# Performance work log

Measured on AMD Instinct MI355X. Metric: run time of the kernel, lower is better.

The kernel has to match this reference:

```python
import jax, jax.numpy as jnp
import numpy as np

V, E, H, L, S, B = 32000, 512, 1024, 2, 512, 32


def setup_inputs() -> dict:
    key = jax.random.key(0)
    ks = jax.random.split(key, 12)
    s = 0.05  # keep activations in a sane range
    return {
        "x": jax.random.randint(ks[0], (S, B), 0, V),
        "embed": jax.random.normal(ks[1], (V, E), dtype=jnp.float32) * s,
        "W_ih0": jax.random.normal(ks[2], (4 * H, E), dtype=jnp.float32) * s,
        "W_hh0": jax.random.normal(ks[3], (4 * H, H), dtype=jnp.float32) * s,
        "b_ih0": jax.random.normal(ks[4], (4 * H,), dtype=jnp.float32) * s,
        "b_hh0": jax.random.normal(ks[5], (4 * H,), dtype=jnp.float32) * s,
        "W_ih1": jax.random.normal(ks[6], (4 * H, H), dtype=jnp.float32) * s,
        "W_hh1": jax.random.normal(ks[7], (4 * H, H), dtype=jnp.float32) * s,
        "b_ih1": jax.random.normal(ks[8], (4 * H,), dtype=jnp.float32) * s,
        "b_hh1": jax.random.normal(ks[9], (4 * H,), dtype=jnp.float32) * s,
        "h0": jax.random.normal(ks[10], (L, B, H), dtype=jnp.float32) * s,
        "c0": jax.random.normal(ks[11], (L, B, H), dtype=jnp.float32) * s,
    }


def _lstm_cell(x_t, h_prev, c_prev, Wi, Wh, bi, bh):
    # PyTorch gate order: input, forget, cell(g), output
    gates = x_t @ Wi.T + h_prev @ Wh.T + bi + bh  # [B, 4H]
    i, f, g, o = jnp.split(gates, 4, axis=-1)
    i = jax.nn.sigmoid(i)
    f = jax.nn.sigmoid(f)
    g = jnp.tanh(g)
    o = jax.nn.sigmoid(o)
    c_new = f * c_prev + i * g
    h_new = o * jnp.tanh(c_new)
    return h_new, c_new


def reference(x, embed, W_ih0, W_hh0, b_ih0, b_hh0,
              W_ih1, W_hh1, b_ih1, b_hh1, h0, c0):
    emb = embed[x]  # [S, B, E]; dropout p=0.0 -> identity
    layers = ((W_ih0, W_hh0, b_ih0, b_hh0), (W_ih1, W_hh1, b_ih1, b_hh1))

    def step(carry, e_t):
        h, c = carry  # each [L, B, H]
        inp = e_t
        new_h, new_c = [], []
        for l, (Wi, Wh, bi, bh) in enumerate(layers):
            h_l, c_l = _lstm_cell(inp, h[l], c[l], Wi, Wh, bi, bh)
            new_h.append(h_l)
            new_c.append(c_l)
            inp = h_l  # inter-layer dropout p=0.0 -> identity
        h = jnp.stack(new_h)
        c = jnp.stack(new_c)
        return (h, c), (inp, h, c)

    (_, _), (outs, hiddens, cells) = jax.lax.scan(step, (h0, c0), emb)
    outputs = outs[:, None, :, :]  # match torch shape [S, 1, B, H]
    return outputs, hiddens, cells
```

## Files before the change

kernel.cpp:

```cpp
#include <hip/hip_runtime.h>
#include <hip/hip_cooperative_groups.h>

namespace cg = cooperative_groups;


#define S_LEN 512
#define BATCH 32
#define HID   1024
#define EMB   512
#define NBLK  128
#define NTHR  512

typedef short  bf16x8 __attribute__((ext_vector_type(8)));
typedef float  f32x4  __attribute__((ext_vector_type(4)));

union U8 { bf16x8 v; unsigned short us[8]; uint4 u4; unsigned long long ull[2]; };

__device__ __forceinline__ unsigned short f2bf(float f) {
    unsigned u = __float_as_uint(f);
    u += 0x7fffu + ((u >> 16) & 1u);
    return (unsigned short)(u >> 16);
}

__device__ __forceinline__ uint4 pack8(float4 lo, float4 hi) {
    U8 r;
    r.us[0] = f2bf(lo.x); r.us[1] = f2bf(lo.y); r.us[2] = f2bf(lo.z); r.us[3] = f2bf(lo.w);
    r.us[4] = f2bf(hi.x); r.us[5] = f2bf(hi.y); r.us[6] = f2bf(hi.z); r.us[7] = f2bf(hi.w);
    return r.u4;
}

__device__ __forceinline__ f32x4 mfma16(bf16x8 a, bf16x8 b, f32x4 c) {
    return __builtin_amdgcn_mfma_f32_16x16x32_bf16(a, b, c, 0, 0, 0);
}

__device__ __forceinline__ U8 ld_ws16(const uint4* p) {
    const unsigned long long* q = (const unsigned long long*)p;
    U8 r;
    r.ull[0] = __hip_atomic_load(q,     __ATOMIC_RELAXED, __HIP_MEMORY_SCOPE_AGENT);
    r.ull[1] = __hip_atomic_load(q + 1, __ATOMIC_RELAXED, __HIP_MEMORY_SCOPE_AGENT);
    return r;
}
__device__ __forceinline__ void st_ws16(uint4* p, U8 v) {
    unsigned long long* q = (unsigned long long*)p;
    __hip_atomic_store(q,     v.ull[0], __ATOMIC_RELAXED, __HIP_MEMORY_SCOPE_AGENT);
    __hip_atomic_store(q + 1, v.ull[1], __ATOMIC_RELAXED, __HIP_MEMORY_SCOPE_AGENT);
}

__device__ __forceinline__ float sigm(float x) {
    return __builtin_amdgcn_rcpf(1.0f + __expf(-x));
}
__device__ __forceinline__ float tanh_fast(float x) {
    const float xc = fminf(fmaxf(x, -15.f), 15.f);
    const float t  = __expf(2.f * xc);
    return (t - 1.f) * __builtin_amdgcn_rcpf(t + 1.f);
}

__device__ __forceinline__ void poll64(const int* flags, int target) {
    const int* p = flags + ((threadIdx.x & 63) << 4);
    for (;;) {
        const int v = __hip_atomic_load(p, __ATOMIC_RELAXED, __HIP_MEMORY_SCOPE_AGENT);
        if (__all(v >= target)) break;
        __builtin_amdgcn_s_sleep(1);
    }
}
__device__ __forceinline__ void pollsub(const int* flags, int base, int cnt, int target) {
    const int l   = threadIdx.x & 63;
    const int idx = (l < cnt) ? l : 0;
    const int* p  = flags + ((base + idx) << 4);
    for (;;) {
        const int v = __hip_atomic_load(p, __ATOMIC_RELAXED, __HIP_MEMORY_SCOPE_AGENT);
        if (__all(v >= target)) break;
        __builtin_amdgcn_s_sleep(1);
    }
}

__global__ __launch_bounds__(NTHR, 1)
void lstm_pipe(const int* __restrict__ x, const float* __restrict__ embed,
               const float* __restrict__ Wi0, const float* __restrict__ Wh0,
               const float* __restrict__ bi0, const float* __restrict__ bh0,
               const float* __restrict__ Wi1, const float* __restrict__ Wh1,
               const float* __restrict__ bi1, const float* __restrict__ bh1,
               const float* __restrict__ h0in, const float* __restrict__ c0in,
               float* __restrict__ outputs, float* __restrict__ hiddens,
               float* __restrict__ cells, uint4* __restrict__ ws)
{
    __shared__ f32x4 sRed[8][8][64];
    __shared__ uint4 sEmb[64 * 33];
    __shared__ float sGates[32][68];
    __shared__ unsigned short sHex[32][16];
    __shared__ float sBias[16][4];

    const int tid  = threadIdx.x;
    const int lane = tid & 63;
    const int wv   = tid >> 6;
    const int bx   = blockIdx.x;
    const bool isL0 = (bx < 64);
    const int g    = isL0 ? bx : bx - 64;

    uint4* h0base = ws;
    uint4* h1base = ws + 16384;
    int*   fbase  = (int*)(ws + 24576);
    int*   flag0  = fbase;
    int*   flag1  = fbase + 1024;

    {
        const int gt = bx * NTHR + tid;
        if (gt < 2048) fbase[gt] = 0;
        if (gt < 8192) {
            const int layer = gt >> 12, kg = (gt >> 5) & 127, b = gt & 31;
            const float* src = h0in + (((size_t)layer << 5) + b) * HID + (kg << 3);
            uint4* dst = layer ? (h1base + 4096) : (h0base + 3 * 4096);
            dst[(kg << 5) + b] = pack8(*(const float4*)src, *(const float4*)(src + 4));
        }
    }
    if (tid < 16) {
        #pragma unroll
        for (int gate = 0; gate < 4; ++gate) {
            const int r = (gate << 10) + (g << 4) + tid;
            sBias[tid][gate] = isL0 ? (bi0[r] + bh0[r]) : (bi1[r] + bh1[r]);
        }
    }
    const int pjj = tid & 15;
    const int pb  = tid >> 4;
    const int jg  = (g << 4) + pjj;
    float creg = isL0 ? c0in[(size_t)pb * HID + jg]
                      : c0in[(size_t)(BATCH + pb) * HID + jg];

    const int n_  = lane & 15;
    const int ko_ = (lane >> 4) << 3;
    const int rb_ = ((n_ >> 2) << 10) + (g << 4) + (n_ & 3);
    bf16x8 w0[4][6];
    bf16x8 w1[4][8];
    if (isL0) {
        #pragma unroll
        for (int nt = 0; nt < 4; ++nt) {
            const int r = rb_ + (nt << 2);
            #pragma unroll
            for (int kf = 0; kf < 6; ++kf) {
                const int k = wv * 192 + kf * 32 + ko_;
                const float* src = (k < EMB) ? Wi0 + (size_t)r * EMB + k
                                             : Wh0 + (size_t)r * HID + (k - EMB);
                U8 t; t.u4 = pack8(*(const float4*)src, *(const float4*)(src + 4));
                w0[nt][kf] = t.v;
            }
        }
    } else {
        #pragma unroll
        for (int nt = 0; nt < 4; ++nt) {
            const int r = rb_ + (nt << 2);
            #pragma unroll
            for (int kf = 0; kf < 8; ++kf) {
                const int k = (wv << 8) + kf * 32 + ko_;
                const float* src = (k < HID) ? Wi1 + (size_t)r * HID + k
                                             : Wh1 + (size_t)r * HID + (k - HID);
                U8 t; t.u4 = pack8(*(const float4*)src, *(const float4*)(src + 4));
                w1[nt][kf] = t.v;
            }
        }
    }

    float4 pe[4][2];
    if (isL0) {
        #pragma unroll
        for (int it = 0; it < 4; ++it) {
            const int b = wv + (it << 3);
            const float* src = embed + (size_t)x[b] * EMB + (lane << 3);
            sEmb[lane * 33 + b] = pack8(*(const float4*)src, *(const float4*)(src + 4));
        }
        #pragma unroll
        for (int it = 0; it < 4; ++it) {
            const int b = wv + (it << 3);
            const float* src = embed + (size_t)x[32 + b] * EMB + (lane << 3);
            pe[it][0] = *(const float4*)src;
            pe[it][1] = *(const float4*)(src + 4);
        }
    }

    cg::grid_group grid = cg::this_grid();
    grid.sync();

    const size_t BH = (size_t)BATCH * HID;

    if (isL0) {
        for (int s = 0; s < S_LEN; ++s) {
            U8 r0[6], r1[6];
            if (wv >= 2) {
                const int fst = (wv * 6 < 16) ? 16 : wv * 6;
                const int pb0 = (fst - 16) << 1;
                const int pct = ((wv * 6 + 6 - 16) << 1) - pb0;
                pollsub(flag0, pb0, pct, s);
                const uint4* h0p = h0base + (((s + 3) & 3) << 12);
                #pragma unroll
                for (int kf = 0; kf < 6; ++kf) {
                    const int kfg = wv * 6 + kf;
                    if (kfg >= 16) {
                        const int u = (((kfg - 16) << 2) + (lane >> 4)) * 32 + (lane & 15);
                        r0[kf] = ld_ws16(&h0p[u]);
                        r1[kf] = ld_ws16(&h0p[u + 16]);
                    }
                }
            }
            f32x4 acc[2][4] = {{{0,0,0,0},{0,0,0,0},{0,0,0,0},{0,0,0,0}},
                               {{0,0,0,0},{0,0,0,0},{0,0,0,0},{0,0,0,0}}};
            #pragma unroll
            for (int kf = 0; kf < 6; ++kf) {
                const int kfg = wv * 6 + kf;
                bf16x8 a0, a1;
                if (kfg < 16) {
                    const int u = ((kfg << 2) + (lane >> 4)) * 33 + (lane & 15);
                    U8 t0; t0.u4 = sEmb[u];      a0 = t0.v;
                    U8 t1; t1.u4 = sEmb[u + 16]; a1 = t1.v;
                } else {
                    a0 = r0[kf].v;
                    a1 = r1[kf].v;
                }
                #pragma unroll
                for (int nt = 0; nt < 4; ++nt) {
                    acc[0][nt] = mfma16(a0, w0[nt][kf], acc[0][nt]);
                    acc[1][nt] = mfma16(a1, w0[nt][kf], acc[1][nt]);
                }
            }
            #pragma unroll
            for (int mt = 0; mt < 2; ++mt)
                #pragma unroll
                for (int nt = 0; nt < 4; ++nt)
                    sRed[wv][(mt << 2) + nt][lane] = acc[mt][nt];
            __syncthreads();

            if (s + 1 < S_LEN) {
                #pragma unroll
                for (int it = 0; it < 4; ++it)
                    sEmb[lane * 33 + wv + (it << 3)] = pack8(pe[it][0], pe[it][1]);
            }
            if (s + 2 < S_LEN) {
                #pragma unroll
                for (int it = 0; it < 4; ++it) {
                    const int b = wv + (it << 3);
                    const float* src = embed + (size_t)x[((s + 2) << 5) + b] * EMB + (lane << 3);
                    pe[it][0] = *(const float4*)src;
                    pe[it][1] = *(const float4*)(src + 4);
                }
            }
            {
                const int tile = tid >> 6, l = tid & 63;
                f32x4 sum = sRed[0][tile][l];
                #pragma unroll
                for (int w = 1; w < 8; ++w) sum += sRed[w][tile][l];
                const int mt = tile >> 2, nt = tile & 3;
                const int b0 = (mt << 4) + ((l >> 4) << 2);
                const int col = (nt << 4) + (l & 15);
                sGates[b0 + 0][col] = sum[0];
                sGates[b0 + 1][col] = sum[1];
                sGates[b0 + 2][col] = sum[2];
                sGates[b0 + 3][col] = sum[3];
            }
            __syncthreads();

            float cn_out, hn_out;
            {
                const int cb = ((pjj >> 2) << 4) + (pjj & 3);
                const float ii = sigm     (sGates[pb][cb]      + sBias[pjj][0]);
                const float ff = sigm     (sGates[pb][cb + 4]  + sBias[pjj][1]);
                const float gg = tanh_fast(sGates[pb][cb + 8]  + sBias[pjj][2]);
                const float oo = sigm     (sGates[pb][cb + 12] + sBias[pjj][3]);
                cn_out = ff * creg + ii * gg;
                creg = cn_out;
                hn_out = oo * tanh_fast(cn_out);
                sHex[pb][pjj] = f2bf(hn_out);
            }
            __syncthreads();

            if (wv == 0) {
                if (s >= 4) poll64(flag1, s - 3);
                const int b = lane & 31, kgl = lane >> 5;
                U8 hb;
                #pragma unroll
                for (int jj = 0; jj < 8; ++jj) hb.us[jj] = sHex[b][(kgl << 3) + jj];
                st_ws16(h0base + ((s & 3) << 12) + (((g << 1) + kgl) << 5) + b, hb);
                asm volatile("s_waitcnt vmcnt(0)" ::: "memory");
                if (lane == 0)
                    __hip_atomic_store(flag0 + (g << 4), s + 1,
                                       __ATOMIC_RELAXED, __HIP_MEMORY_SCOPE_AGENT);
            }
            cells  [(size_t)(s << 1) * BH + (size_t)pb * HID + jg] = cn_out;
            hiddens[(size_t)(s << 1) * BH + (size_t)pb * HID + jg] = hn_out;
        }
    } else {
        for (int s = 0; s < S_LEN; ++s) {
            if (wv < 4) pollsub(flag0, wv << 4, 16, s + 1);
            else        poll64(flag1, s);

            const uint4* h0c = h0base + ((s & 3) << 12);
            const uint4* h1p = h1base + (((s + 1) & 1) << 12);
            U8 r0[8], r1[8];
            #pragma unroll
            for (int kf = 0; kf < 8; ++kf) {
                const int kfg = (wv << 3) + kf;
                const uint4* src = (kfg < 32) ? h0c : h1p;
                const int u = (((kfg & 31) << 2) + (lane >> 4)) * 32 + (lane & 15);
                r0[kf] = ld_ws16(&src[u]);
                r1[kf] = ld_ws16(&src[u + 16]);
            }
            f32x4 acc[2][4] = {{{0,0,0,0},{0,0,0,0},{0,0,0,0},{0,0,0,0}},
                               {{0,0,0,0},{0,0,0,0},{0,0,0,0},{0,0,0,0}}};
            #pragma unroll
            for (int kf = 0; kf < 8; ++kf) {
                #pragma unroll
                for (int nt = 0; nt < 4; ++nt) {
                    acc[0][nt] = mfma16(r0[kf].v, w1[nt][kf], acc[0][nt]);
                    acc[1][nt] = mfma16(r1[kf].v, w1[nt][kf], acc[1][nt]);
                }
            }
            #pragma unroll
            for (int mt = 0; mt < 2; ++mt)
                #pragma unroll
                for (int nt = 0; nt < 4; ++nt)
                    sRed[wv][(mt << 2) + nt][lane] = acc[mt][nt];
            __syncthreads();
            {
                const int tile = tid >> 6, l = tid & 63;
                f32x4 sum = sRed[0][tile][l];
                #pragma unroll
                for (int w = 1; w < 8; ++w) sum += sRed[w][tile][l];
                const int mt = tile >> 2, nt = tile & 3;
                const int b0 = (mt << 4) + ((l >> 4) << 2);
                const int col = (nt << 4) + (l & 15);
                sGates[b0 + 0][col] = sum[0];
                sGates[b0 + 1][col] = sum[1];
                sGates[b0 + 2][col] = sum[2];
                sGates[b0 + 3][col] = sum[3];
            }
            __syncthreads();
            float cn_out, hn_out;
            {
                const int cb = ((pjj >> 2) << 4) + (pjj & 3);
                const float ii = sigm     (sGates[pb][cb]      + sBias[pjj][0]);
                const float ff = sigm     (sGates[pb][cb + 4]  + sBias[pjj][1]);
                const float gg = tanh_fast(sGates[pb][cb + 8]  + sBias[pjj][2]);
                const float oo = sigm     (sGates[pb][cb + 12] + sBias[pjj][3]);
                cn_out = ff * creg + ii * gg;
                creg = cn_out;
                hn_out = oo * tanh_fast(cn_out);
                sHex[pb][pjj] = f2bf(hn_out);
            }
            __syncthreads();
            if (wv == 0) {
                const int b = lane & 31, kgl = lane >> 5;
                U8 hb;
                #pragma unroll
                for (int jj = 0; jj < 8; ++jj) hb.us[jj] = sHex[b][(kgl << 3) + jj];
                st_ws16(h1base + ((s & 1) << 12) + (((g << 1) + kgl) << 5) + b, hb);
                asm volatile("s_waitcnt vmcnt(0)" ::: "memory");
                if (lane == 0)
                    __hip_atomic_store(flag1 + (g << 4), s + 1,
                                       __ATOMIC_RELAXED, __HIP_MEMORY_SCOPE_AGENT);
            }
            {
                const size_t o = (size_t)pb * HID + jg;
                cells  [(size_t)((s << 1) + 1) * BH + o] = cn_out;
                hiddens[(size_t)((s << 1) + 1) * BH + o] = hn_out;
                outputs[(size_t)s * BH + o]              = hn_out;
            }
        }
    }
}

#define KC 256
__global__ __launch_bounds__(256)
void lstm_step(const float* __restrict__ Wi, const float* __restrict__ Wh,
               const float* __restrict__ bi, const float* __restrict__ bh,
               const float* __restrict__ xsrc, const int* __restrict__ xidx, int K1,
               const float* __restrict__ Hprev, const float* __restrict__ Cprev,
               float* __restrict__ Hout, float* __restrict__ Cout,
               float* __restrict__ Hout2)
{
    __shared__ float As[32][KC + 4];
    __shared__ float red[256][5];

    const int t  = threadIdx.x;
    const int b  = t & 31;
    const int jl = (t >> 5) & 1;
    const int ks = t >> 6;
    const int j  = (blockIdx.x << 1) + jl;

    const int Ktot = K1 + HID;
    const int NC   = Ktot / KC;

    float acc0 = 0.f, acc1 = 0.f, acc2 = 0.f, acc3 = 0.f;

    for (int c = 0; c < NC; ++c) {
        const int  k0  = c * KC;
        const bool isX = (k0 < K1);

        #pragma unroll
        for (int i = 0; i < 8; ++i) {
            const int idx4 = t + (i << 8);
            const int row  = idx4 >> 6;
            const int c4   = idx4 & 63;
            const float* src;
            if (isX) {
                const size_t r0 = xidx ? (size_t)xidx[row] : (size_t)row;
                src = xsrc + r0 * (size_t)K1 + k0;
            } else {
                src = Hprev + (size_t)row * HID + (k0 - K1);
            }
            *(float4*)&As[row][c4 << 2] = *(const float4*)(src + (c4 << 2));
        }
        __syncthreads();

        const float* W      = isX ? Wi : Wh;
        const int    stride = isX ? K1 : HID;
        const int    kw     = k0 + (ks << 6) - (isX ? 0 : K1);
        const float* w0 = W + (size_t)(j       ) * stride + kw;
        const float* w1 = W + (size_t)(j + 1024) * stride + kw;
        const float* w2 = W + (size_t)(j + 2048) * stride + kw;
        const float* w3 = W + (size_t)(j + 3072) * stride + kw;
        const float* a  = &As[b][ks << 6];

        #pragma unroll 4
        for (int kk = 0; kk < 64; kk += 4) {
            const float4 av = *(const float4*)(a + kk);
            float4 w;
            w = *(const float4*)(w0 + kk);
            acc0 = fmaf(av.x, w.x, acc0); acc0 = fmaf(av.y, w.y, acc0);
            acc0 = fmaf(av.z, w.z, acc0); acc0 = fmaf(av.w, w.w, acc0);
            w = *(const float4*)(w1 + kk);
            acc1 = fmaf(av.x, w.x, acc1); acc1 = fmaf(av.y, w.y, acc1);
            acc1 = fmaf(av.z, w.z, acc1); acc1 = fmaf(av.w, w.w, acc1);
            w = *(const float4*)(w2 + kk);
            acc2 = fmaf(av.x, w.x, acc2); acc2 = fmaf(av.y, w.y, acc2);
            acc2 = fmaf(av.z, w.z, acc2); acc2 = fmaf(av.w, w.w, acc2);
            w = *(const float4*)(w3 + kk);
            acc3 = fmaf(av.x, w.x, acc3); acc3 = fmaf(av.y, w.y, acc3);
            acc3 = fmaf(av.z, w.z, acc3); acc3 = fmaf(av.w, w.w, acc3);
        }
        __syncthreads();
    }

    red[t][0] = acc0; red[t][1] = acc1; red[t][2] = acc2; red[t][3] = acc3;
    __syncthreads();

    if (t < 64) {
        float tot[4];
        #pragma unroll
        for (int gg = 0; gg < 4; ++gg) {
            const int r = j + (gg << 10);
            tot[gg] = red[t][gg] + red[t + 64][gg] + red[t + 128][gg] + red[t + 192][gg]
                   + bi[r] + bh[r];
        }
        const float ig = 1.f / (1.f + expf(-tot[0]));
        const float fg = 1.f / (1.f + expf(-tot[1]));
        const float gv = tanhf(tot[2]);
        const float og = 1.f / (1.f + expf(-tot[3]));
        const size_t o  = (size_t)b * HID + j;
        const float  cp = Cprev[o];
        const float  cn = fg * cp + ig * gv;
        const float  hn = og * tanhf(cn);
        Cout[o] = cn;
        Hout[o] = hn;
        if (Hout2) Hout2[o] = hn;
    }
}

extern "C" void kernel_launch(void* const* d_in, const int* in_sizes, int n_in,
                              void* d_out, int out_size, void* d_ws, size_t ws_size,
                              hipStream_t stream)
{
    (void)in_sizes; (void)n_in; (void)out_size;

    const int*   x     = (const int*)  d_in[0];
    const float* embed = (const float*)d_in[1];
    const float* Wi0   = (const float*)d_in[2];
    const float* Wh0   = (const float*)d_in[3];
    const float* bi0   = (const float*)d_in[4];
    const float* bh0   = (const float*)d_in[5];
    const float* Wi1   = (const float*)d_in[6];
    const float* Wh1   = (const float*)d_in[7];
    const float* bi1   = (const float*)d_in[8];
    const float* bh1   = (const float*)d_in[9];
    const float* h0in  = (const float*)d_in[10];
    const float* c0in  = (const float*)d_in[11];

    float* out     = (float*)d_out;
    const size_t BH = (size_t)BATCH * HID;
    float* outputs = out;
    float* hiddens = out + (size_t)S_LEN * BH;
    float* cells   = out + 3 * (size_t)S_LEN * BH;
    uint4* ws      = (uint4*)d_ws;

    bool coop_ok = (ws_size >= 401408);
    if (coop_ok) {
        void* args[] = {
            (void*)&x, (void*)&embed,
            (void*)&Wi0, (void*)&Wh0, (void*)&bi0, (void*)&bh0,
            (void*)&Wi1, (void*)&Wh1, (void*)&bi1, (void*)&bh1,
            (void*)&h0in, (void*)&c0in,
            (void*)&outputs, (void*)&hiddens, (void*)&cells, (void*)&ws
        };
        hipError_t e = hipLaunchCooperativeKernel((void*)lstm_pipe,
                                                  dim3(NBLK), dim3(NTHR), args, 0, stream);
        if (e != hipSuccess) { (void)hipGetLastError(); coop_ok = false; }
    }
    if (!coop_ok) {
        for (int s = 0; s < S_LEN; ++s) {
            const float* Hp0 = s ? hiddens + ((size_t)(s - 1) * 2 + 0) * BH : h0in;
            const float* Cp0 = s ? cells   + ((size_t)(s - 1) * 2 + 0) * BH : c0in;
            float* H0o = hiddens + ((size_t)s * 2 + 0) * BH;
            float* C0o = cells   + ((size_t)s * 2 + 0) * BH;
            lstm_step<<<512, 256, 0, stream>>>(Wi0, Wh0, bi0, bh0,
                                               embed, x + (size_t)s * BATCH, EMB,
                                               Hp0, Cp0, H0o, C0o, nullptr);

            const float* Hp1 = s ? hiddens + ((size_t)(s - 1) * 2 + 1) * BH : h0in + BH;
            const float* Cp1 = s ? cells   + ((size_t)(s - 1) * 2 + 1) * BH : c0in + BH;
            float* H1o = hiddens + ((size_t)s * 2 + 1) * BH;
            float* C1o = cells   + ((size_t)s * 2 + 1) * BH;
            lstm_step<<<512, 256, 0, stream>>>(Wi1, Wh1, bi1, bh1,
                                               H0o, nullptr, HID,
                                               Hp1, Cp1, H1o, C1o, outputs + (size_t)s * BH);
        }
    }
}
```

Baseline: 3.361 ms.

## Split batch into two independent 128-block pipelines of 16 rows each

Doubles the cooperative grid to 256 blocks and splits the batch into two independent groups of 16 rows. Each group runs its own layer-0/layer-1 pipeline with separate workspace buffers and flags. Per-block MFMA work, LDS use and per-step h loads are halved, which shortens the serial per-step critical path. In exchange each block duplicates the full weight-register load, and half the threads idle during the gate stage. The cooperative launch also needs 256 co-resident blocks.

Result: faster. 2.910 ms, median of 2 (-13.4%).

```diff
diff --git a/kernel.cpp b/kernel.cpp
--- a/kernel.cpp
+++ b/kernel.cpp
@@ -8,7 +8,7 @@
 #define BATCH 32
 #define HID   1024
 #define EMB   512
-#define NBLK  128
+#define NBLK  256
 #define NTHR  512
 
 typedef short  bf16x8 __attribute__((ext_vector_type(8)));
@@ -84,33 +84,36 @@
                float* __restrict__ outputs, float* __restrict__ hiddens,
                float* __restrict__ cells, uint4* __restrict__ ws)
 {
-    __shared__ f32x4 sRed[8][8][64];
-    __shared__ uint4 sEmb[64 * 33];
-    __shared__ float sGates[32][68];
-    __shared__ unsigned short sHex[32][16];
+    __shared__ f32x4 sRed[8][4][64];
+    __shared__ uint4 sEmb[64 * 17];
+    __shared__ float sGates[16][68];
+    __shared__ unsigned short sHex[16][16];
     __shared__ float sBias[16][4];
 
     const int tid  = threadIdx.x;
     const int lane = tid & 63;
     const int wv   = tid >> 6;
     const int bx   = blockIdx.x;
-    const bool isL0 = (bx < 64);
-    const int g    = isL0 ? bx : bx - 64;
-
-    uint4* h0base = ws;
-    uint4* h1base = ws + 16384;
-    int*   fbase  = (int*)(ws + 24576);
+    const int grp  = bx >> 7;
+    const int gbx  = bx & 127;
+    const bool isL0 = (gbx < 64);
+    const int g    = isL0 ? gbx : gbx - 64;
+
+    uint4* h0base = ws + grp * 12288;
+    uint4* h1base = h0base + 8192;
+    int*   fbase  = (int*)(ws + 24576) + grp * 2048;
     int*   flag0  = fbase;
     int*   flag1  = fbase + 1024;
 
     {
         const int gt = bx * NTHR + tid;
-        if (gt < 2048) fbase[gt] = 0;
+        if (gt < 4096) ((int*)(ws + 24576))[gt] = 0;
         if (gt < 8192) {
-            const int layer = gt >> 12, kg = (gt >> 5) & 127, b = gt & 31;
-            const float* src = h0in + (((size_t)layer << 5) + b) * HID + (kg << 3);
-            uint4* dst = layer ? (h1base + 4096) : (h0base + 3 * 4096);
-            dst[(kg << 5) + b] = pack8(*(const float4*)src, *(const float4*)(src + 4));
+            const int b = gt & 15, kg8 = (gt >> 4) & 127;
+            const int layer = (gt >> 11) & 1, gg = gt >> 12;
+            const float* src = h0in + ((size_t)((layer << 5) + (gg << 4) + b)) * HID + (kg8 << 3);
+            uint4* dst = ws + gg * 12288 + (layer ? (8192 + 2048) : (3 * 2048));
+            dst[(kg8 << 4) + b] = pack8(*(const float4*)src, *(const float4*)(src + 4));
         }
     }
     if (tid < 16) {
@@ -121,10 +124,12 @@
         }
     }
     const int pjj = tid & 15;
-    const int pb  = tid >> 4;
+    const int pb  = (tid >> 4) & 15;
     const int jg  = (g << 4) + pjj;
-    float creg = isL0 ? c0in[(size_t)pb * HID + jg]
-                      : c0in[(size_t)(BATCH + pb) * HID + jg];
+    const int growbase = (grp << 4);
+    float creg = 0.f;
+    if (tid < 256)
+        creg = c0in[(size_t)((isL0 ? 0 : BATCH) + growbase + pb) * HID + jg];
 
     const int n_  = lane & 15;
     const int ko_ = (lane >> 4) << 3;
@@ -159,18 +164,18 @@
         }
     }
 
-    float4 pe[4][2];
+    float4 pe[2][2];
     if (isL0) {
         #pragma unroll
-        for (int it = 0; it < 4; ++it) {
+        for (int it = 0; it < 2; ++it) {
             const int b = wv + (it << 3);
-            const float* src = embed + (size_t)x[b] * EMB + (lane << 3);
-            sEmb[lane * 33 + b] = pack8(*(const float4*)src, *(const float4*)(src + 4));
-        }
-        #pragma unroll
-        for (int it = 0; it < 4; ++it) {
+            const float* src = embed + (size_t)x[growbase + b] * EMB + (lane << 3);
+            sEmb[lane * 17 + b] = pack8(*(const float4*)src, *(const float4*)(src + 4));
+        }
+        #pragma unroll
+        for (int it = 0; it < 2; ++it) {
             const int b = wv + (it << 3);
-            const float* src = embed + (size_t)x[32 + b] * EMB + (lane << 3);
+            const float* src = embed + (size_t)x[32 + growbase + b] * EMB + (lane << 3);
             pe[it][0] = *(const float4*)src;
             pe[it][1] = *(const float4*)(src + 4);
         }
@@ -183,71 +188,62 @@
 
     if (isL0) {
         for (int s = 0; s < S_LEN; ++s) {
-            U8 r0[6], r1[6];
+            U8 r0[6];
             if (wv >= 2) {
                 const int fst = (wv * 6 < 16) ? 16 : wv * 6;
                 const int pb0 = (fst - 16) << 1;
                 const int pct = ((wv * 6 + 6 - 16) << 1) - pb0;
                 pollsub(flag0, pb0, pct, s);
-                const uint4* h0p = h0base + (((s + 3) & 3) << 12);
+                const uint4* h0p = h0base + (((s + 3) & 3) << 11);
                 #pragma unroll
                 for (int kf = 0; kf < 6; ++kf) {
                     const int kfg = wv * 6 + kf;
                     if (kfg >= 16) {
-                        const int u = (((kfg - 16) << 2) + (lane >> 4)) * 32 + (lane & 15);
+                        const int u = ((((kfg - 16) << 2) + (lane >> 4)) << 4) + (lane & 15);
                         r0[kf] = ld_ws16(&h0p[u]);
-                        r1[kf] = ld_ws16(&h0p[u + 16]);
                     }
                 }
             }
-            f32x4 acc[2][4] = {{{0,0,0,0},{0,0,0,0},{0,0,0,0},{0,0,0,0}},
-                               {{0,0,0,0},{0,0,0,0},{0,0,0,0},{0,0,0,0}}};
+            f32x4 acc[4] = {{0,0,0,0},{0,0,0,0},{0,0,0,0},{0,0,0,0}};
             #pragma unroll
             for (int kf = 0; kf < 6; ++kf) {
                 const int kfg = wv * 6 + kf;
-                bf16x8 a0, a1;
+                bf16x8 a0;
                 if (kfg < 16) {
-                    const int u = ((kfg << 2) + (lane >> 4)) * 33 + (lane & 15);
-                    U8 t0; t0.u4 = sEmb[u];      a0 = t0.v;
-                    U8 t1; t1.u4 = sEmb[u + 16]; a1 = t1.v;
+                    const int u = ((kfg << 2) + (lane >> 4)) * 17 + (lane & 15);
+                    U8 t0; t0.u4 = sEmb[u]; a0 = t0.v;
                 } else {
                     a0 = r0[kf].v;
-                    a1 = r1[kf].v;
                 }
                 #pragma unroll
-                for (int nt = 0; nt < 4; ++nt) {
-                    acc[0][nt] = mfma16(a0, w0[nt][kf], acc[0][nt]);
-                    acc[1][nt] = mfma16(a1, w0[nt][kf], acc[1][nt]);
-                }
-            }
-            #pragma unroll
-            for (int mt = 0; mt < 2; ++mt)
-                #pragma unroll
                 for (int nt = 0; nt < 4; ++nt)
-                    sRed[wv][(mt << 2) + nt][lane] = acc[mt][nt];
+                    acc[nt] = mfma16(a0, w0[nt][kf], acc[nt]);
+            }
+            #pragma unroll
+            for (int nt = 0; nt < 4; ++nt)
+                sRed[wv][nt][lane] = acc[nt];
             __syncthreads();
 
             if (s + 1 < S_LEN) {
                 #pragma unroll
-                for (int it = 0; it < 4; ++it)
-                    sEmb[lane * 33 + wv + (it << 3)] = pack8(pe[it][0], pe[it][1]);
+                for (int it = 0; it < 2; ++it)
+                    sEmb[lane * 17 + wv + (it << 3)] = pack8(pe[it][0], pe[it][1]);
             }
             if (s + 2 < S_LEN) {
                 #pragma unroll
-                for (int it = 0; it < 4; ++it) {
+                for (int it = 0; it < 2; ++it) {
                     const int b = wv + (it << 3);
-                    const float* src = embed + (size_t)x[((s + 2) << 5) + b] * EMB + (lane << 3);
+                    const float* src = embed + (size_t)x[((s + 2) << 5) + growbase + b] * EMB + (lane << 3);
                     pe[it][0] = *(const float4*)src;
                     pe[it][1] = *(const float4*)(src + 4);
                 }
             }
-            {
-                const int tile = tid >> 6, l = tid & 63;
-                f32x4 sum = sRed[0][tile][l];
-                #pragma unroll
-                for (int w = 1; w < 8; ++w) sum += sRed[w][tile][l];
-                const int mt = tile >> 2, nt = tile & 3;
-                const int b0 = (mt << 4) + ((l >> 4) << 2);
+            if (tid < 256) {
+                const int nt = tid >> 6, l = tid & 63;
+                f32x4 sum = sRed[0][nt][l];
+                #pragma unroll
+                for (int w = 1; w < 8; ++w) sum += sRed[w][nt][l];
+                const int b0 = (l >> 4) << 2;
                 const int col = (nt << 4) + (l & 15);
                 sGates[b0 + 0][col] = sum[0];
                 sGates[b0 + 1][col] = sum[1];
@@ -256,8 +252,8 @@
             }
             __syncthreads();
 
-            float cn_out, hn_out;
-            {
+            float cn_out = 0.f, hn_out = 0.f;
+            if (tid < 256) {
                 const int cb = ((pjj >> 2) << 4) + (pjj & 3);
                 const float ii = sigm     (sGates[pb][cb]      + sBias[pjj][0]);
                 const float ff = sigm     (sGates[pb][cb + 4]  + sBias[pjj][1]);
@@ -272,58 +268,56 @@
 
             if (wv == 0) {
                 if (s >= 4) poll64(flag1, s - 3);
-                const int b = lane & 31, kgl = lane >> 5;
-                U8 hb;
-                #pragma unroll
-                for (int jj = 0; jj < 8; ++jj) hb.us[jj] = sHex[b][(kgl << 3) + jj];
-                st_ws16(h0base + ((s & 3) << 12) + (((g << 1) + kgl) << 5) + b, hb);
+                if (lane < 32) {
+                    const int b = lane & 15, kgl = lane >> 4;
+                    U8 hb;
+                    #pragma unroll
+                    for (int jj = 0; jj < 8; ++jj) hb.us[jj] = sHex[b][(kgl << 3) + jj];
+                    st_ws16(h0base + ((s & 3) << 11) + ((((g << 1) + kgl)) << 4) + b, hb);
+                }
                 asm volatile("s_waitcnt vmcnt(0)" ::: "memory");
                 if (lane == 0)
                     __hip_atomic_store(flag0 + (g << 4), s + 1,
                                        __ATOMIC_RELAXED, __HIP_MEMORY_SCOPE_AGENT);
             }
-            cells  [(size_t)(s << 1) * BH + (size_t)pb * HID + jg] = cn_out;
-            hiddens[(size_t)(s << 1) * BH + (size_t)pb * HID + jg] = hn_out;
+            if (tid < 256) {
+                const size_t o = (size_t)(growbase + pb) * HID + jg;
+                cells  [(size_t)(s << 1) * BH + o] = cn_out;
+                hiddens[(size_t)(s << 1) * BH + o] = hn_out;
+            }
         }
     } else {
         for (int s = 0; s < S_LEN; ++s) {
             if (wv < 4) pollsub(flag0, wv << 4, 16, s + 1);
             else        poll64(flag1, s);
 
-            const uint4* h0c = h0base + ((s & 3) << 12);
-            const uint4* h1p = h1base + (((s + 1) & 1) << 12);
-            U8 r0[8], r1[8];
+            const uint4* h0c = h0base + ((s & 3) << 11);
+            const uint4* h1p = h1base + (((s + 1) & 1) << 11);
+            U8 r0[8];
             #pragma unroll
             for (int kf = 0; kf < 8; ++kf) {
                 const int kfg = (wv << 3) + kf;
                 const uint4* src = (kfg < 32) ? h0c : h1p;
-                const int u = (((kfg & 31) << 2) + (lane >> 4)) * 32 + (lane & 15);
+                const int u = ((((kfg & 31) << 2) + (lane >> 4)) << 4) + (lane & 15);
                 r0[kf] = ld_ws16(&src[u]);
-                r1[kf] = ld_ws16(&src[u + 16]);
-            }
-            f32x4 acc[2][4] = {{{0,0,0,0},{0,0,0,0},{0,0,0,0},{0,0,0,0}},
-                               {{0,0,0,0},{0,0,0,0},{0,0,0,0},{0,0,0,0}}};
+            }
+            f32x4 acc[4] = {{0,0,0,0},{0,0,0,0},{0,0,0,0},{0,0,0,0}};
             #pragma unroll
             for (int kf = 0; kf < 8; ++kf) {
                 #pragma unroll
-                for (int nt = 0; nt < 4; ++nt) {
-                    acc[0][nt] = mfma16(r0[kf].v, w1[nt][kf], acc[0][nt]);
-                    acc[1][nt] = mfma16(r1[kf].v, w1[nt][kf], acc[1][nt]);
-                }
-            }
-            #pragma unroll
-            for (int mt = 0; mt < 2; ++mt)
-                #pragma unroll
                 for (int nt = 0; nt < 4; ++nt)
-                    sRed[wv][(mt << 2) + nt][lane] = acc[mt][nt];
+                    acc[nt] = mfma16(r0[kf].v, w1[nt][kf], acc[nt]);
+            }
+            #pragma unroll
+            for (int nt = 0; nt < 4; ++nt)
+                sRed[wv][nt][lane] = acc[nt];
             __syncthreads();
-            {
-                const int tile = tid >> 6, l = tid & 63;
-                f32x4 sum = sRed[0][tile][l];
-                #pragma unroll
-                for (int w = 1; w < 8; ++w) sum += sRed[w][tile][l];
-                const int mt = tile >> 2, nt = tile & 3;
-                const int b0 = (mt << 4) + ((l >> 4) << 2);
+            if (tid < 256) {
+                const int nt = tid >> 6, l = tid & 63;
+                f32x4 sum = sRed[0][nt][l];
+                #pragma unroll
+                for (int w = 1; w < 8; ++w) sum += sRed[w][nt][l];
+                const int b0 = (l >> 4) << 2;
                 const int col = (nt << 4) + (l & 15);
                 sGates[b0 + 0][col] = sum[0];
                 sGates[b0 + 1][col] = sum[1];
@@ -331,8 +325,8 @@
                 sGates[b0 + 3][col] = sum[3];
             }
             __syncthreads();
-            float cn_out, hn_out;
-            {
+            float cn_out = 0.f, hn_out = 0.f;
+            if (tid < 256) {
                 const int cb = ((pjj >> 2) << 4) + (pjj & 3);
                 const float ii = sigm     (sGates[pb][cb]      + sBias[pjj][0]);
                 const float ff = sigm     (sGates[pb][cb + 4]  + sBias[pjj][1]);
@@ -345,18 +339,20 @@
             }
             __syncthreads();
             if (wv == 0) {
-                const int b = lane & 31, kgl = lane >> 5;
-                U8 hb;
-                #pragma unroll
-                for (int jj = 0; jj < 8; ++jj) hb.us[jj] = sHex[b][(kgl << 3) + jj];
-                st_ws16(h1base + ((s & 1) << 12) + (((g << 1) + kgl) << 5) + b, hb);
+                if (lane < 32) {
+                    const int b = lane & 15, kgl = lane >> 4;
+                    U8 hb;
+                    #pragma unroll
+                    for (int jj = 0; jj < 8; ++jj) hb.us[jj] = sHex[b][(kgl << 3) + jj];
+                    st_ws16(h1base + ((s & 1) << 11) + ((((g << 1) + kgl)) << 4) + b, hb);
+                }
                 asm volatile("s_waitcnt vmcnt(0)" ::: "memory");
                 if (lane == 0)
                     __hip_atomic_store(flag1 + (g << 4), s + 1,
                                        __ATOMIC_RELAXED, __HIP_MEMORY_SCOPE_AGENT);
             }
-            {
-                const size_t o = (size_t)pb * HID + jg;
+            if (tid < 256) {
+                const size_t o = (size_t)(growbase + pb) * HID + jg;
                 cells  [(size_t)((s << 1) + 1) * BH + o] = cn_out;
                 hiddens[(size_t)((s << 1) + 1) * BH + o] = hn_out;
                 outputs[(size_t)s * BH + o]              = hn_out;
@@ -488,7 +484,7 @@
     float* cells   = out + 3 * (size_t)S_LEN * BH;
     uint4* ws      = (uint4*)d_ws;
 
-    bool coop_ok = (ws_size >= 401408);
+    bool coop_ok = (ws_size >= 409600);
     if (coop_ok) {
         void* args[] = {
             (void*)&x, (void*)&embed,
```
